# Optimization experiments

Measured on AMD Instinct MI355X. Metric: run time of the kernel, lower is better.

## Reference

```python
import itertools
import jax, jax.numpy as jnp
import numpy as np

B = 1024      # graphs
N = 40        # atoms per graph (module supports 1..49)
ETA = 64
K = 32        # num_clusters
ZD = 32       # z_dim
NA = 10       # num_atom_types
NB = 5        # num_bond_types + 1
CH, AH, BH = 128, 128, 64
TAU = 1.0


def _resblock(x, W1, b1, W2, b2, Ws, bs):
    # assumed ResidualBlock: Linear->ReLU->(dropout, eval=identity)->Linear + linear skip
    h = jax.nn.relu(x @ W1 + b1)
    return h @ W2 + b2 + (x @ Ws + bs)


def setup_inputs() -> dict:
    key = jax.random.key(0)
    ks = jax.random.split(key, 24)
    s = 0.05
    pairs = np.array(list(itertools.combinations(range(N), 2)), dtype=np.int32)  # [780,2]
    offsets = (np.arange(B, dtype=np.int32) * N)[:, None, None]
    edge_index = jnp.asarray((pairs[None] + offsets).reshape(-1, 2))  # [B*780, 2]
    return {
        "eta": jax.random.normal(ks[0], (B, ETA), jnp.float32),
        "gumbel_noise": jax.random.gumbel(ks[1], (B * N, K), jnp.float32),
        "z_noise": jax.random.normal(ks[2], (B * N, ZD), jnp.float32),
        "cW1": jax.random.normal(ks[3], (ETA, CH)) * s, "cb1": jnp.zeros((CH,)),
        "cW2": jax.random.normal(ks[4], (CH, K)) * s, "cb2": jnp.zeros((K,)),
        "cWs": jax.random.normal(ks[5], (ETA, K)) * s, "cbs": jnp.zeros((K,)),
        "cluster_means": jax.random.normal(ks[6], (K, ZD)),
        "cluster_log_sigmas": jnp.full((K, ZD), -2.0),
        "aW1": jax.random.normal(ks[7], (ZD, AH)) * s, "ab1": jnp.zeros((AH,)),
        "aW2": jax.random.normal(ks[8], (AH, NA)) * s, "ab2": jnp.zeros((NA,)),
        "aWs": jax.random.normal(ks[9], (ZD, NA)) * s, "abs_": jnp.zeros((NA,)),
        "bond_matrix": jax.random.normal(ks[10], (NB, ZD, ZD)),
        "bW1": jax.random.normal(ks[11], (NB, BH)) * s, "bb1": jnp.zeros((BH,)),
        "bW2": jax.random.normal(ks[12], (BH, NB)) * s, "bb2": jnp.zeros((NB,)),
        "bWs": jax.random.normal(ks[13], (NB, NB)) * s, "bbs": jnp.zeros((NB,)),
        "edge_index": edge_index,
    }


def reference(eta, gumbel_noise, z_noise,
              cW1, cb1, cW2, cb2, cWs, cbs,
              cluster_means, cluster_log_sigmas,
              aW1, ab1, aW2, ab2, aWs, abs_,
              bond_matrix, bW1, bb1, bW2, bb2, bWs, bbs,
              edge_index):
    # decode_eta: mixture weights
    pi = jax.nn.softmax(_resblock(eta, cW1, cb1, cW2, cb2, cWs, cbs), axis=1)  # [B,K]
    log_pi = jnp.log(pi)
    # sample_c: gumbel-softmax (hard, straight-through) per node
    logits = jnp.repeat(log_pi, N, axis=0)                      # [B*N, K]
    y_soft = jax.nn.softmax((logits + gumbel_noise) / TAU, axis=-1)
    y_hard = jax.nn.one_hot(jnp.argmax(y_soft, axis=-1), K, dtype=y_soft.dtype)
    c = y_hard + y_soft - jax.lax.stop_gradient(y_soft)         # straight-through
    # sample_z
    mu = c @ cluster_means                                      # [B*N, ZD]
    log_sigma = c @ cluster_log_sigmas
    sigma = jnp.exp(jnp.clip(log_sigma, -20.0, 30.0))
    z = z_noise * sigma + mu
    # decode_z: atom logits
    atom_types = _resblock(z, aW1, ab1, aW2, ab2, aWs, abs_)    # [B*N, NA]
    # symmetrized per-bond-type bilinear form over edge node pairs
    Wsym = 0.5 * (bond_matrix + jnp.swapaxes(bond_matrix, 1, 2))  # [NB, ZD, ZD]
    zi = z[edge_index[:, 0]]                                    # [E, ZD]
    zj = z[edge_index[:, 1]]                                    # [E, ZD]
    bil = jnp.einsum('ed,tdc,ec->et', zi, Wsym, zj)             # [E, NB]
    edge_logits = _resblock(bil, bW1, bb1, bW2, bb2, bWs, bbs)
    edge_types = jax.nn.softmax(edge_logits, axis=1)            # [E, NB]
    return atom_types, edge_types
```

## Files before the change

kernel.cpp:

```cpp
#include <hip/hip_runtime.h>

constexpr int NPAIR = 780, NA = 10;
constexpr int ZTP = 44;
constexpr int WSR = 36, WSP = 1156, UTP = 1408;
constexpr int OFF_ZT = 0;
constexpr int OFF_A  = 1408;
constexpr int OFF_HT = OFF_A;
constexpr int OFF_WS = OFF_A;
constexpr int OFF_UT = OFF_A + 5 * WSP;
constexpr int OFF_BT = OFF_A;
constexpr int OFF_HW = OFF_A + 5 * 784;
constexpr int OFF_ET = 14228;
constexpr int OFF_HC = 14292;
constexpr int OFF_LP = 14420;
constexpr int SH_TOT = 14452;

__global__ __launch_bounds__(256, 2) void fused_kernel(
    const float* __restrict__ eta, const float* __restrict__ gumbel,
    const float* __restrict__ z_noise,
    const float* __restrict__ cW1, const float* __restrict__ cb1,
    const float* __restrict__ cW2, const float* __restrict__ cb2,
    const float* __restrict__ cWs, const float* __restrict__ cbs,
    const float* __restrict__ means, const float* __restrict__ lsig,
    const float* __restrict__ aW1, const float* __restrict__ ab1,
    const float* __restrict__ aW2, const float* __restrict__ ab2,
    const float* __restrict__ aWs, const float* __restrict__ abs_,
    const float* __restrict__ bond,
    const float* __restrict__ bW1, const float* __restrict__ bb1,
    const float* __restrict__ bW2, const float* __restrict__ bb2,
    const float* __restrict__ bWs, const float* __restrict__ bbs,
    float* __restrict__ atom_out, float* __restrict__ edge_out)
{
  __shared__ __align__(16) float S[SH_TOT];
  const int tid = threadIdx.x;
  const int m = blockIdx.x;

  if (tid < 64) S[OFF_ET + tid] = eta[m * 64 + tid];
  __syncthreads();

  if (tid < 128) {
    float h = cb1[tid];
    #pragma unroll 8
    for (int d = 0; d < 64; ++d) h += S[OFF_ET + d] * cW1[d * 128 + tid];
    S[OFF_HC + tid] = fmaxf(h, 0.f);
  }
  __syncthreads();

  if (tid < 32) {
    float x = cb2[tid] + cbs[tid];
    #pragma unroll 8
    for (int j = 0; j < 128; ++j) x += S[OFF_HC + j] * cW2[j * 32 + tid];
    #pragma unroll 8
    for (int d = 0; d < 64; ++d)  x += S[OFF_ET + d] * cWs[d * 32 + tid];
    float mx = x;
    for (int off = 16; off; off >>= 1) mx = fmaxf(mx, __shfl_xor(mx, off));
    float e = __expf(x - mx);
    float s = e;
    for (int off = 16; off; off >>= 1) s += __shfl_xor(s, off);
    S[OFF_LP + tid] = (x - mx) - __logf(s);
  }
  __syncthreads();

  if (tid < 40) {
    const int n = m * 40 + tid;
    float g[32];
    const float4* g4 = (const float4*)(gumbel + (size_t)n * 32);
    #pragma unroll
    for (int q = 0; q < 8; ++q) {
      float4 v = g4[q];
      g[4*q] = v.x; g[4*q+1] = v.y; g[4*q+2] = v.z; g[4*q+3] = v.w;
    }
    int kb = 0; float vb = S[OFF_LP] + g[0];
    #pragma unroll
    for (int c = 1; c < 32; ++c) {
      float v = S[OFF_LP + c] + g[c];
      if (v > vb) { vb = v; kb = c; }
    }
    const float4* zn4 = (const float4*)(z_noise + (size_t)n * 32);
    const float4* mk4 = (const float4*)(means + kb * 32);
    const float4* ls4 = (const float4*)(lsig + kb * 32);
    #pragma unroll
    for (int q = 0; q < 8; ++q) {
      float4 zn = zn4[q], mk = mk4[q], ls = ls4[q];
      float z0 = zn.x * __expf(fminf(fmaxf(ls.x, -20.f), 30.f)) + mk.x;
      float z1 = zn.y * __expf(fminf(fmaxf(ls.y, -20.f), 30.f)) + mk.y;
      float z2 = zn.z * __expf(fminf(fmaxf(ls.z, -20.f), 30.f)) + mk.z;
      float z3 = zn.w * __expf(fminf(fmaxf(ls.w, -20.f), 30.f)) + mk.w;
      S[OFF_ZT + (4*q    ) * ZTP + tid] = z0;
      S[OFF_ZT + (4*q + 1) * ZTP + tid] = z1;
      S[OFF_ZT + (4*q + 2) * ZTP + tid] = z2;
      S[OFF_ZT + (4*q + 3) * ZTP + tid] = z3;
    }
  }
  __syncthreads();

  for (int u = tid; u < 320; u += 256) {
    const int ng = u >> 5, jg = u & 31;
    const int n0 = ng * 4, j0 = jg * 4;
    float acc[4][4];
    #pragma unroll
    for (int a = 0; a < 4; ++a)
      #pragma unroll
      for (int b = 0; b < 4; ++b) acc[a][b] = 0.f;
    #pragma unroll 8
    for (int c = 0; c < 32; ++c) {
      float4 zv = *(const float4*)&S[OFF_ZT + c * ZTP + n0];
      float4 wv = *(const float4*)(aW1 + c * 128 + j0);
      acc[0][0] += zv.x * wv.x; acc[0][1] += zv.x * wv.y; acc[0][2] += zv.x * wv.z; acc[0][3] += zv.x * wv.w;
      acc[1][0] += zv.y * wv.x; acc[1][1] += zv.y * wv.y; acc[1][2] += zv.y * wv.z; acc[1][3] += zv.y * wv.w;
      acc[2][0] += zv.z * wv.x; acc[2][1] += zv.z * wv.y; acc[2][2] += zv.z * wv.z; acc[2][3] += zv.z * wv.w;
      acc[3][0] += zv.w * wv.x; acc[3][1] += zv.w * wv.y; acc[3][2] += zv.w * wv.z; acc[3][3] += zv.w * wv.w;
    }
    float4 bv = *(const float4*)(ab1 + j0);
    float bj[4] = {bv.x, bv.y, bv.z, bv.w};
    #pragma unroll
    for (int b = 0; b < 4; ++b) {
      float4 hv;
      hv.x = fmaxf(acc[0][b] + bj[b], 0.f);
      hv.y = fmaxf(acc[1][b] + bj[b], 0.f);
      hv.z = fmaxf(acc[2][b] + bj[b], 0.f);
      hv.w = fmaxf(acc[3][b] + bj[b], 0.f);
      *(float4*)&S[OFF_HT + (j0 + b) * ZTP + n0] = hv;
    }
  }
  __syncthreads();

  if (tid < 200) {
    const int n = tid / 5, kp = tid - (tid / 5) * 5, k0 = kp * 2;
    float a0 = ab2[k0] + abs_[k0];
    float a1 = ab2[k0 + 1] + abs_[k0 + 1];
    #pragma unroll 8
    for (int c = 0; c < 32; ++c) {
      float zc = S[OFF_ZT + c * ZTP + n];
      float2 w = *(const float2*)(aWs + c * 10 + k0);
      a0 += zc * w.x; a1 += zc * w.y;
    }
    #pragma unroll 8
    for (int j = 0; j < 128; ++j) {
      float hv = S[OFF_HT + j * ZTP + n];
      float2 w = *(const float2*)(aW2 + j * 10 + k0);
      a0 += hv * w.x; a1 += hv * w.y;
    }
    atom_out[(size_t)m * 400 + n * 10 + k0]     = a0;
    atom_out[(size_t)m * 400 + n * 10 + k0 + 1] = a1;
  }
  __syncthreads();

  for (int e = tid; e < 5120; e += 256) {
    int t = e >> 10, r = e & 1023, c = r >> 5, d = r & 31;
    S[OFF_WS + t * WSP + c * WSR + d] =
        0.5f * (bond[t * 1024 + c * 32 + d] + bond[t * 1024 + d * 32 + c]);
  }
  __syncthreads();

  for (int u = tid; u < 400; u += 256) {
    const int t = u / 80, r = u - t * 80;
    const int dg = r / 10, ig = r - dg * 10;
    const int d0 = dg * 4, i0 = ig * 4;
    float acc[4][4];
    #pragma unroll
    for (int a = 0; a < 4; ++a)
      #pragma unroll
      for (int b = 0; b < 4; ++b) acc[a][b] = 0.f;
    #pragma unroll 8
    for (int c = 0; c < 32; ++c) {
      float4 zv = *(const float4*)&S[OFF_ZT + c * ZTP + i0];
      float4 wv = *(const float4*)&S[OFF_WS + t * WSP + c * WSR + d0];
      acc[0][0] += wv.x * zv.x; acc[0][1] += wv.x * zv.y; acc[0][2] += wv.x * zv.z; acc[0][3] += wv.x * zv.w;
      acc[1][0] += wv.y * zv.x; acc[1][1] += wv.y * zv.y; acc[1][2] += wv.y * zv.z; acc[1][3] += wv.y * zv.w;
      acc[2][0] += wv.z * zv.x; acc[2][1] += wv.z * zv.y; acc[2][2] += wv.z * zv.z; acc[2][3] += wv.z * zv.w;
      acc[3][0] += wv.w * zv.x; acc[3][1] += wv.w * zv.y; acc[3][2] += wv.w * zv.z; acc[3][3] += wv.w * zv.w;
    }
    #pragma unroll
    for (int a = 0; a < 4; ++a)
      *(float4*)&S[OFF_UT + t * UTP + (d0 + a) * ZTP + i0] =
          make_float4(acc[a][0], acc[a][1], acc[a][2], acc[a][3]);
  }
  __syncthreads();

  if (tid < 150) {
    const int t = tid / 30, q = tid - t * 30;
    int ig, jg;
    if (q < 10)      { ig = 0; jg = q; }
    else if (q < 18) { ig = 1; jg = q - 8; }
    else if (q < 24) { ig = 2; jg = q - 14; }
    else if (q < 28) { ig = 3; jg = q - 18; }
    else             { ig = 4; jg = q - 20; }
    const int i0 = ig * 8, j0 = jg * 4;
    float acc[8][4];
    #pragma unroll
    for (int a = 0; a < 8; ++a)
      #pragma unroll
      for (int b = 0; b < 4; ++b) acc[a][b] = 0.f;
    #pragma unroll 4
    for (int d = 0; d < 32; ++d) {
      float4 u0 = *(const float4*)&S[OFF_UT + t * UTP + d * ZTP + i0];
      float4 u1 = *(const float4*)&S[OFF_UT + t * UTP + d * ZTP + i0 + 4];
      float4 zv = *(const float4*)&S[OFF_ZT + d * ZTP + j0];
      float ua[8] = {u0.x,u0.y,u0.z,u0.w,u1.x,u1.y,u1.z,u1.w};
      #pragma unroll
      for (int a = 0; a < 8; ++a) {
        acc[a][0] += ua[a] * zv.x; acc[a][1] += ua[a] * zv.y;
        acc[a][2] += ua[a] * zv.z; acc[a][3] += ua[a] * zv.w;
      }
    }
    #pragma unroll
    for (int a = 0; a < 8; ++a) {
      const int i = i0 + a;
      #pragma unroll
      for (int b = 0; b < 4; ++b) {
        const int j = j0 + b;
        if (i < j) {
          const int p = i * (79 - i) / 2 + (j - i - 1);
          S[OFF_BT + t * 784 + p] = acc[a][b];
        }
      }
    }
  } else {
    for (int idx = tid - 150; idx < 744; idx += 106) {
      float v;
      if (idx < 320) v = bW1[idx];
      else if (idx < 384) v = bb1[idx - 320];
      else if (idx < 704) { int qq = idx - 384; int t2 = qq >> 6, j = qq & 63; v = bW2[j * 5 + t2];
                            S[OFF_HW + 384 + t2 * 64 + j] = v; continue; }
      else if (idx < 709) v = bb2[idx - 704];
      else if (idx < 734) v = bWs[idx - 709];
      else v = bbs[idx - 734];
      S[OFF_HW + idx] = v;
    }
  }
  __syncthreads();

  const float* w1h = &S[OFF_HW];
  const float* b1h = &S[OFF_HW + 320];
  const float* w2t = &S[OFF_HW + 384];
  const float* b2h = &S[OFF_HW + 704];
  const float* wsh = &S[OFF_HW + 709];
  const float* bsh = &S[OFF_HW + 734];

  float bil5[4][5], lg[4][5];
  #pragma unroll
  for (int s = 0; s < 4; ++s) {
    const int p = tid + (s << 8);
    const int pc = (p < NPAIR) ? p : 0;
    #pragma unroll
    for (int t = 0; t < 5; ++t) bil5[s][t] = S[OFF_BT + t * 784 + pc];
    #pragma unroll
    for (int t2 = 0; t2 < 5; ++t2) {
      float a = b2h[t2] + bsh[t2];
      #pragma unroll
      for (int t = 0; t < 5; ++t) a += bil5[s][t] * wsh[t * 5 + t2];
      lg[s][t2] = a;
    }
  }
  for (int j4 = 0; j4 < 16; ++j4) {
    float4 bb = ((const float4*)b1h)[j4];
    float4 w1v[5], w2v[5];
    #pragma unroll
    for (int t = 0; t < 5; ++t) {
      w1v[t] = ((const float4*)(w1h + t * 64))[j4];
      w2v[t] = ((const float4*)(w2t + t * 64))[j4];
    }
    #pragma unroll
    for (int s = 0; s < 4; ++s) {
      float4 h = bb;
      #pragma unroll
      for (int t = 0; t < 5; ++t) {
        float bt = bil5[s][t];
        h.x += bt * w1v[t].x; h.y += bt * w1v[t].y; h.z += bt * w1v[t].z; h.w += bt * w1v[t].w;
      }
      h.x = fmaxf(h.x, 0.f); h.y = fmaxf(h.y, 0.f); h.z = fmaxf(h.z, 0.f); h.w = fmaxf(h.w, 0.f);
      #pragma unroll
      for (int t2 = 0; t2 < 5; ++t2)
        lg[s][t2] += h.x * w2v[t2].x + h.y * w2v[t2].y + h.z * w2v[t2].z + h.w * w2v[t2].w;
    }
  }
  #pragma unroll
  for (int s = 0; s < 4; ++s) {
    const int p = tid + (s << 8);
    if (p >= NPAIR) continue;
    float mx = lg[s][0];
    #pragma unroll
    for (int t2 = 1; t2 < 5; ++t2) mx = fmaxf(mx, lg[s][t2]);
    float e[5], sum = 0.f;
    #pragma unroll
    for (int t2 = 0; t2 < 5; ++t2) { e[t2] = __expf(lg[s][t2] - mx); sum += e[t2]; }
    float inv = 1.f / sum;
    float* outp = edge_out + ((size_t)m * NPAIR + p) * 5;
    #pragma unroll
    for (int t2 = 0; t2 < 5; ++t2) outp[t2] = e[t2] * inv;
  }
}

extern "C" void kernel_launch(void* const* d_in, const int* in_sizes, int n_in,
                              void* d_out, int out_size, void* d_ws, size_t ws_size,
                              hipStream_t stream) {
  const float* eta    = (const float*)d_in[0];
  const float* gumbel = (const float*)d_in[1];
  const float* z_noise= (const float*)d_in[2];
  const float* cW1 = (const float*)d_in[3];
  const float* cb1 = (const float*)d_in[4];
  const float* cW2 = (const float*)d_in[5];
  const float* cb2 = (const float*)d_in[6];
  const float* cWs = (const float*)d_in[7];
  const float* cbs = (const float*)d_in[8];
  const float* means = (const float*)d_in[9];
  const float* lsig  = (const float*)d_in[10];
  const float* aW1 = (const float*)d_in[11];
  const float* ab1 = (const float*)d_in[12];
  const float* aW2 = (const float*)d_in[13];
  const float* ab2 = (const float*)d_in[14];
  const float* aWs = (const float*)d_in[15];
  const float* abs_= (const float*)d_in[16];
  const float* bond= (const float*)d_in[17];
  const float* bW1 = (const float*)d_in[18];
  const float* bb1 = (const float*)d_in[19];
  const float* bW2 = (const float*)d_in[20];
  const float* bb2 = (const float*)d_in[21];
  const float* bWs = (const float*)d_in[22];
  const float* bbs = (const float*)d_in[23];

  float* atom_out = (float*)d_out;
  float* edge_out = atom_out + (size_t)1024 * 400;

  fused_kernel<<<1024, 256, 0, stream>>>(eta, gumbel, z_noise,
                                         cW1, cb1, cW2, cb2, cWs, cbs,
                                         means, lsig, aW1, ab1, aW2, ab2, aWs, abs_,
                                         bond, bW1, bb1, bW2, bb2, bWs, bbs,
                                         atom_out, edge_out);
}
```

Baseline: 211.1 us.

## Precompute symmetric bond weights and sigma in prep kernel, shrink LDS for occupancy

Adds a small prep kernel that builds the symmetrised bond matrices and the clamped exp of the cluster log-sigmas once, rather than in every block. The fused kernel reads Wsym directly from global memory, so it no longer stages it in shared memory. It also processes the bond planes in two rounds (3 then 2) to shrink the UT buffer, and cuts the LDS footprint so it can raise launch bounds to 4 blocks per CU. The edge-MLP weight staging moves to idle threads in the first stage, and the hidden-layer loop is reordered to reduce register pressure. The costs are an extra launch, a workspace dependency, and an extra barrier pair per block.

```diff
diff --git a/kernel.cpp b/kernel.cpp
--- a/kernel.cpp
+++ b/kernel.cpp
@@ -1,31 +1,45 @@
 #include <hip/hip_runtime.h>
 
-constexpr int NPAIR = 780, NA = 10;
-constexpr int ZTP = 44;
-constexpr int WSR = 36, WSP = 1156, UTP = 1408;
+constexpr int NPAIR = 780;
+
+constexpr int ZTP    = 40;
 constexpr int OFF_ZT = 0;
-constexpr int OFF_A  = 1408;
+constexpr int OFF_A  = 1280;
 constexpr int OFF_HT = OFF_A;
-constexpr int OFF_WS = OFF_A;
-constexpr int OFF_UT = OFF_A + 5 * WSP;
-constexpr int OFF_BT = OFF_A;
-constexpr int OFF_HW = OFF_A + 5 * 784;
-constexpr int OFF_ET = 14228;
-constexpr int OFF_HC = 14292;
-constexpr int OFF_LP = 14420;
-constexpr int SH_TOT = 14452;
-
-__global__ __launch_bounds__(256, 2) void fused_kernel(
+constexpr int OFF_UT = OFF_A;
+constexpr int UTP    = 1280;
+constexpr int OFF_BT = OFF_A + 3840;
+constexpr int OFF_HW = OFF_BT + 3900;
+constexpr int OFF_ET = OFF_HW + 744;
+constexpr int OFF_HC = OFF_ET + 64;
+constexpr int OFF_LP = OFF_HC + 128;
+constexpr int SH_TOT = OFF_LP + 32;
+
+__global__ __launch_bounds__(256) void prep_kernel(
+    const float* __restrict__ bond, const float* __restrict__ lsig,
+    float* __restrict__ wsym, float* __restrict__ sigma)
+{
+  const int e = blockIdx.x * 256 + threadIdx.x;
+  if (e < 5120) {
+    const int t = e >> 10, r = e & 1023, c = r >> 5, d = r & 31;
+    wsym[e] = 0.5f * (bond[e] + bond[t * 1024 + d * 32 + c]);
+  } else if (e < 6144) {
+    const int q = e - 5120;
+    sigma[q] = __expf(fminf(fmaxf(lsig[q], -20.f), 30.f));
+  }
+}
+
+__global__ __launch_bounds__(256, 4) void fused_kernel(
     const float* __restrict__ eta, const float* __restrict__ gumbel,
     const float* __restrict__ z_noise,
     const float* __restrict__ cW1, const float* __restrict__ cb1,
     const float* __restrict__ cW2, const float* __restrict__ cb2,
     const float* __restrict__ cWs, const float* __restrict__ cbs,
-    const float* __restrict__ means, const float* __restrict__ lsig,
+    const float* __restrict__ means, const float* __restrict__ sigma,
     const float* __restrict__ aW1, const float* __restrict__ ab1,
     const float* __restrict__ aW2, const float* __restrict__ ab2,
     const float* __restrict__ aWs, const float* __restrict__ abs_,
-    const float* __restrict__ bond,
+    const float* __restrict__ wsym,
     const float* __restrict__ bW1, const float* __restrict__ bb1,
     const float* __restrict__ bW2, const float* __restrict__ bb2,
     const float* __restrict__ bWs, const float* __restrict__ bbs,
@@ -43,6 +57,18 @@
     #pragma unroll 8
     for (int d = 0; d < 64; ++d) h += S[OFF_ET + d] * cW1[d * 128 + tid];
     S[OFF_HC + tid] = fmaxf(h, 0.f);
+  } else {
+    for (int idx = tid - 128; idx < 739; idx += 128) {
+      float v;
+      if (idx < 320) v = bW1[idx];
+      else if (idx < 384) v = bb1[idx - 320];
+      else if (idx < 704) { int qq = idx - 384; int t2 = qq >> 6, j = qq & 63;
+                            S[OFF_HW + 384 + t2 * 64 + j] = bW2[j * 5 + t2]; continue; }
+      else if (idx < 709) v = bb2[idx - 704];
+      else if (idx < 734) v = bWs[idx - 709];
+      else v = bbs[idx - 734];
+      S[OFF_HW + idx] = v;
+    }
   }
   __syncthreads();
 
@@ -78,18 +104,14 @@
     }
     const float4* zn4 = (const float4*)(z_noise + (size_t)n * 32);
     const float4* mk4 = (const float4*)(means + kb * 32);
-    const float4* ls4 = (const float4*)(lsig + kb * 32);
+    const float4* sg4 = (const float4*)(sigma + kb * 32);
     #pragma unroll
     for (int q = 0; q < 8; ++q) {
-      float4 zn = zn4[q], mk = mk4[q], ls = ls4[q];
-      float z0 = zn.x * __expf(fminf(fmaxf(ls.x, -20.f), 30.f)) + mk.x;
-      float z1 = zn.y * __expf(fminf(fmaxf(ls.y, -20.f), 30.f)) + mk.y;
-      float z2 = zn.z * __expf(fminf(fmaxf(ls.z, -20.f), 30.f)) + mk.z;
-      float z3 = zn.w * __expf(fminf(fmaxf(ls.w, -20.f), 30.f)) + mk.w;
-      S[OFF_ZT + (4*q    ) * ZTP + tid] = z0;
-      S[OFF_ZT + (4*q + 1) * ZTP + tid] = z1;
-      S[OFF_ZT + (4*q + 2) * ZTP + tid] = z2;
-      S[OFF_ZT + (4*q + 3) * ZTP + tid] = z3;
+      float4 zn = zn4[q], mk = mk4[q], sg = sg4[q];
+      S[OFF_ZT + (4*q    ) * ZTP + tid] = zn.x * sg.x + mk.x;
+      S[OFF_ZT + (4*q + 1) * ZTP + tid] = zn.y * sg.y + mk.y;
+      S[OFF_ZT + (4*q + 2) * ZTP + tid] = zn.z * sg.z + mk.z;
+      S[OFF_ZT + (4*q + 3) * ZTP + tid] = zn.w * sg.w + mk.w;
     }
   }
   __syncthreads();
@@ -120,7 +142,7 @@
       hv.y = fmaxf(acc[1][b] + bj[b], 0.f);
       hv.z = fmaxf(acc[2][b] + bj[b], 0.f);
       hv.w = fmaxf(acc[3][b] + bj[b], 0.f);
-      *(float4*)&S[OFF_HT + (j0 + b) * ZTP + n0] = hv;
+      *(float4*)&S[OFF_HT + (j0 + b) * 44 + n0] = hv;
     }
   }
   __syncthreads();
@@ -137,99 +159,86 @@
     }
     #pragma unroll 8
     for (int j = 0; j < 128; ++j) {
-      float hv = S[OFF_HT + j * ZTP + n];
+      float hv = S[OFF_HT + j * 44 + n];
       float2 w = *(const float2*)(aW2 + j * 10 + k0);
       a0 += hv * w.x; a1 += hv * w.y;
     }
-    atom_out[(size_t)m * 400 + n * 10 + k0]     = a0;
-    atom_out[(size_t)m * 400 + n * 10 + k0 + 1] = a1;
-  }
-  __syncthreads();
-
-  for (int e = tid; e < 5120; e += 256) {
-    int t = e >> 10, r = e & 1023, c = r >> 5, d = r & 31;
-    S[OFF_WS + t * WSP + c * WSR + d] =
-        0.5f * (bond[t * 1024 + c * 32 + d] + bond[t * 1024 + d * 32 + c]);
-  }
-  __syncthreads();
-
-  for (int u = tid; u < 400; u += 256) {
-    const int t = u / 80, r = u - t * 80;
-    const int dg = r / 10, ig = r - dg * 10;
-    const int d0 = dg * 4, i0 = ig * 4;
-    float acc[4][4];
-    #pragma unroll
-    for (int a = 0; a < 4; ++a)
-      #pragma unroll
-      for (int b = 0; b < 4; ++b) acc[a][b] = 0.f;
-    #pragma unroll 8
-    for (int c = 0; c < 32; ++c) {
-      float4 zv = *(const float4*)&S[OFF_ZT + c * ZTP + i0];
-      float4 wv = *(const float4*)&S[OFF_WS + t * WSP + c * WSR + d0];
-      acc[0][0] += wv.x * zv.x; acc[0][1] += wv.x * zv.y; acc[0][2] += wv.x * zv.z; acc[0][3] += wv.x * zv.w;
-      acc[1][0] += wv.y * zv.x; acc[1][1] += wv.y * zv.y; acc[1][2] += wv.y * zv.z; acc[1][3] += wv.y * zv.w;
-      acc[2][0] += wv.z * zv.x; acc[2][1] += wv.z * zv.y; acc[2][2] += wv.z * zv.z; acc[2][3] += wv.z * zv.w;
-      acc[3][0] += wv.w * zv.x; acc[3][1] += wv.w * zv.y; acc[3][2] += wv.w * zv.z; acc[3][3] += wv.w * zv.w;
-    }
-    #pragma unroll
-    for (int a = 0; a < 4; ++a)
-      *(float4*)&S[OFF_UT + t * UTP + (d0 + a) * ZTP + i0] =
-          make_float4(acc[a][0], acc[a][1], acc[a][2], acc[a][3]);
-  }
-  __syncthreads();
-
-  if (tid < 150) {
-    const int t = tid / 30, q = tid - t * 30;
-    int ig, jg;
-    if (q < 10)      { ig = 0; jg = q; }
-    else if (q < 18) { ig = 1; jg = q - 8; }
-    else if (q < 24) { ig = 2; jg = q - 14; }
-    else if (q < 28) { ig = 3; jg = q - 18; }
-    else             { ig = 4; jg = q - 20; }
-    const int i0 = ig * 8, j0 = jg * 4;
-    float acc[8][4];
-    #pragma unroll
-    for (int a = 0; a < 8; ++a)
-      #pragma unroll
-      for (int b = 0; b < 4; ++b) acc[a][b] = 0.f;
-    #pragma unroll 4
-    for (int d = 0; d < 32; ++d) {
-      float4 u0 = *(const float4*)&S[OFF_UT + t * UTP + d * ZTP + i0];
-      float4 u1 = *(const float4*)&S[OFF_UT + t * UTP + d * ZTP + i0 + 4];
-      float4 zv = *(const float4*)&S[OFF_ZT + d * ZTP + j0];
-      float ua[8] = {u0.x,u0.y,u0.z,u0.w,u1.x,u1.y,u1.z,u1.w};
-      #pragma unroll
-      for (int a = 0; a < 8; ++a) {
-        acc[a][0] += ua[a] * zv.x; acc[a][1] += ua[a] * zv.y;
-        acc[a][2] += ua[a] * zv.z; acc[a][3] += ua[a] * zv.w;
+    *(float2*)(atom_out + (size_t)m * 400 + n * 10 + k0) = make_float2(a0, a1);
+  }
+  __syncthreads();
+
+  #pragma unroll
+  for (int R = 0; R < 2; ++R) {
+    const int tbase = (R == 0) ? 0 : 3;
+    const int nplanes = (R == 0) ? 3 : 2;
+    for (int u = tid; u < nplanes * 80; u += 256) {
+      const int tl = u / 80, r = u - tl * 80;
+      const int dg = r / 10, ig = r - dg * 10;
+      const int d0 = dg * 4, i0 = ig * 4;
+      const float* wg = wsym + (tbase + tl) * 1024;
+      float acc[4][4];
+      #pragma unroll
+      for (int a = 0; a < 4; ++a)
+        #pragma unroll
+        for (int b = 0; b < 4; ++b) acc[a][b] = 0.f;
+      #pragma unroll 8
+      for (int c = 0; c < 32; ++c) {
+        float4 zv = *(const float4*)&S[OFF_ZT + c * ZTP + i0];
+        float4 wv = *(const float4*)(wg + c * 32 + d0);
+        acc[0][0] += wv.x * zv.x; acc[0][1] += wv.x * zv.y; acc[0][2] += wv.x * zv.z; acc[0][3] += wv.x * zv.w;
+        acc[1][0] += wv.y * zv.x; acc[1][1] += wv.y * zv.y; acc[1][2] += wv.y * zv.z; acc[1][3] += wv.y * zv.w;
+        acc[2][0] += wv.z * zv.x; acc[2][1] += wv.z * zv.y; acc[2][2] += wv.z * zv.z; acc[2][3] += wv.z * zv.w;
+        acc[3][0] += wv.w * zv.x; acc[3][1] += wv.w * zv.y; acc[3][2] += wv.w * zv.z; acc[3][3] += wv.w * zv.w;
       }
-    }
-    #pragma unroll
-    for (int a = 0; a < 8; ++a) {
-      const int i = i0 + a;
-      #pragma unroll
-      for (int b = 0; b < 4; ++b) {
-        const int j = j0 + b;
-        if (i < j) {
-          const int p = i * (79 - i) / 2 + (j - i - 1);
-          S[OFF_BT + t * 784 + p] = acc[a][b];
+      #pragma unroll
+      for (int a = 0; a < 4; ++a)
+        *(float4*)&S[OFF_UT + tl * UTP + (d0 + a) * ZTP + i0] =
+            make_float4(acc[a][0], acc[a][1], acc[a][2], acc[a][3]);
+    }
+    __syncthreads();
+
+    if (tid < nplanes * 30) {
+      const int tl = tid / 30, q = tid - tl * 30;
+      const int tg = tbase + tl;
+      int ig, jg;
+      if (q < 10)      { ig = 0; jg = q; }
+      else if (q < 18) { ig = 1; jg = q - 8; }
+      else if (q < 24) { ig = 2; jg = q - 14; }
+      else if (q < 28) { ig = 3; jg = q - 18; }
+      else             { ig = 4; jg = q - 20; }
+      const int i0 = ig * 8, j0 = jg * 4;
+      float acc[8][4];
+      #pragma unroll
+      for (int a = 0; a < 8; ++a)
+        #pragma unroll
+        for (int b = 0; b < 4; ++b) acc[a][b] = 0.f;
+      #pragma unroll 4
+      for (int d = 0; d < 32; ++d) {
+        float4 u0 = *(const float4*)&S[OFF_UT + tl * UTP + d * ZTP + i0];
+        float4 u1 = *(const float4*)&S[OFF_UT + tl * UTP + d * ZTP + i0 + 4];
+        float4 zv = *(const float4*)&S[OFF_ZT + d * ZTP + j0];
+        float ua[8] = {u0.x,u0.y,u0.z,u0.w,u1.x,u1.y,u1.z,u1.w};
+        #pragma unroll
+        for (int a = 0; a < 8; ++a) {
+          acc[a][0] += ua[a] * zv.x; acc[a][1] += ua[a] * zv.y;
+          acc[a][2] += ua[a] * zv.z; acc[a][3] += ua[a] * zv.w;
         }
       }
-    }
-  } else {
-    for (int idx = tid - 150; idx < 744; idx += 106) {
-      float v;
-      if (idx < 320) v = bW1[idx];
-      else if (idx < 384) v = bb1[idx - 320];
-      else if (idx < 704) { int qq = idx - 384; int t2 = qq >> 6, j = qq & 63; v = bW2[j * 5 + t2];
-                            S[OFF_HW + 384 + t2 * 64 + j] = v; continue; }
-      else if (idx < 709) v = bb2[idx - 704];
-      else if (idx < 734) v = bWs[idx - 709];
-      else v = bbs[idx - 734];
-      S[OFF_HW + idx] = v;
-    }
-  }
-  __syncthreads();
+      #pragma unroll
+      for (int a = 0; a < 8; ++a) {
+        const int i = i0 + a;
+        #pragma unroll
+        for (int b = 0; b < 4; ++b) {
+          const int j = j0 + b;
+          if (i < j) {
+            const int p = i * (79 - i) / 2 + (j - i - 1);
+            S[OFF_BT + tg * 780 + p] = acc[a][b];
+          }
+        }
+      }
+    }
+    __syncthreads();
+  }
 
   const float* w1h = &S[OFF_HW];
   const float* b1h = &S[OFF_HW + 320];
@@ -244,7 +253,7 @@
     const int p = tid + (s << 8);
     const int pc = (p < NPAIR) ? p : 0;
     #pragma unroll
-    for (int t = 0; t < 5; ++t) bil5[s][t] = S[OFF_BT + t * 784 + pc];
+    for (int t = 0; t < 5; ++t) bil5[s][t] = S[OFF_BT + t * 780 + pc];
     #pragma unroll
     for (int t2 = 0; t2 < 5; ++t2) {
       float a = b2h[t2] + bsh[t2];
@@ -255,24 +264,29 @@
   }
   for (int j4 = 0; j4 < 16; ++j4) {
     float4 bb = ((const float4*)b1h)[j4];
-    float4 w1v[5], w2v[5];
+    float4 h[4];
+    #pragma unroll
+    for (int s = 0; s < 4; ++s) h[s] = bb;
     #pragma unroll
     for (int t = 0; t < 5; ++t) {
-      w1v[t] = ((const float4*)(w1h + t * 64))[j4];
-      w2v[t] = ((const float4*)(w2t + t * 64))[j4];
+      float4 w1 = ((const float4*)(w1h + t * 64))[j4];
+      #pragma unroll
+      for (int s = 0; s < 4; ++s) {
+        float bt = bil5[s][t];
+        h[s].x += bt * w1.x; h[s].y += bt * w1.y; h[s].z += bt * w1.z; h[s].w += bt * w1.w;
+      }
     }
     #pragma unroll
     for (int s = 0; s < 4; ++s) {
-      float4 h = bb;
-      #pragma unroll
-      for (int t = 0; t < 5; ++t) {
-        float bt = bil5[s][t];
-        h.x += bt * w1v[t].x; h.y += bt * w1v[t].y; h.z += bt * w1v[t].z; h.w += bt * w1v[t].w;
-      }
-      h.x = fmaxf(h.x, 0.f); h.y = fmaxf(h.y, 0.f); h.z = fmaxf(h.z, 0.f); h.w = fmaxf(h.w, 0.f);
-      #pragma unroll
-      for (int t2 = 0; t2 < 5; ++t2)
-        lg[s][t2] += h.x * w2v[t2].x + h.y * w2v[t2].y + h.z * w2v[t2].z + h.w * w2v[t2].w;
+      h[s].x = fmaxf(h[s].x, 0.f); h[s].y = fmaxf(h[s].y, 0.f);
+      h[s].z = fmaxf(h[s].z, 0.f); h[s].w = fmaxf(h[s].w, 0.f);
+    }
+    #pragma unroll
+    for (int t2 = 0; t2 < 5; ++t2) {
+      float4 w2 = ((const float4*)(w2t + t2 * 64))[j4];
+      #pragma unroll
+      for (int s = 0; s < 4; ++s)
+        lg[s][t2] += h[s].x * w2.x + h[s].y * w2.y + h[s].z * w2.z + h[s].w * w2.w;
     }
   }
   #pragma unroll
@@ -320,12 +334,15 @@
   const float* bWs = (const float*)d_in[22];
   const float* bbs = (const float*)d_in[23];
 
+  float* wsym  = (float*)d_ws;
+  float* sigma = wsym + 5120;
   float* atom_out = (float*)d_out;
   float* edge_out = atom_out + (size_t)1024 * 400;
 
+  prep_kernel<<<24, 256, 0, stream>>>(bond, lsig, wsym, sigma);
   fused_kernel<<<1024, 256, 0, stream>>>(eta, gumbel, z_noise,
                                          cW1, cb1, cW2, cb2, cWs, cbs,
-                                         means, lsig, aW1, ab1, aW2, ab2, aWs, abs_,
-                                         bond, bW1, bb1, bW2, bb2, bWs, bbs,
+                                         means, sigma, aW1, ab1, aW2, ab2, aWs, abs_,
+                                         wsym, bW1, bb1, bW2, bb2, bWs, bbs,
                                          atom_out, edge_out);
 }
```

Result: faster. 195.5 us (-7.4%).
